# Kernel optimization log

Hardware: AMD Instinct MI355X
Metric: run time of the kernel (lower is better)

Reference implementation:

```python
import jax, jax.numpy as jnp
import numpy as np

EMBED_DIM = 1024
NUM_HEADS = 16
HEAD_DIM = EMBED_DIM // NUM_HEADS
SCALING = HEAD_DIM ** -0.5
TGT_LEN = 2048
BSZ = 2


def setup_inputs() -> dict:
    key = jax.random.key(0)
    ks = jax.random.split(key, 8)
    E = EMBED_DIM
    query = jax.random.normal(ks[0], (TGT_LEN, BSZ, E), dtype=jnp.float32)
    k_in = jax.random.normal(ks[1], (TGT_LEN, BSZ, E), dtype=jnp.float32)
    v_in = jax.random.normal(ks[2], (TGT_LEN, BSZ, E), dtype=jnp.float32)
    attn_mask = jnp.zeros((TGT_LEN, TGT_LEN), dtype=jnp.float32)
    key_padding_mask = jnp.zeros((1, TGT_LEN, TGT_LEN), dtype=jnp.int32)
    # torch.nn.Linear params: y = x @ W.T + b
    lim_qkv = 1.0 / np.sqrt(E)
    W_qkv = jax.random.uniform(ks[3], (3 * E, E), minval=-lim_qkv, maxval=lim_qkv, dtype=jnp.float32)
    b_qkv = jax.random.uniform(ks[4], (3 * E,), minval=-lim_qkv, maxval=lim_qkv, dtype=jnp.float32)
    W_out = jax.random.uniform(ks[5], (E, E), minval=-lim_qkv, maxval=lim_qkv, dtype=jnp.float32)
    b_out = jax.random.uniform(ks[6], (E,), minval=-lim_qkv, maxval=lim_qkv, dtype=jnp.float32)
    return {"query": query, "key": k_in, "value": v_in, "attn_mask": attn_mask,
            "key_padding_mask": key_padding_mask, "W_qkv": W_qkv, "b_qkv": b_qkv,
            "W_out": W_out, "b_out": b_out}


def reference(query, key, value, attn_mask, key_padding_mask, W_qkv, b_qkv, W_out, b_out):
    # NOTE: original module ignores `key`/`value` args (self-attn from query only).
    T, B, E = query.shape
    H, hd = NUM_HEADS, HEAD_DIM
    neg_inf = jnp.float32(-jnp.inf)
    qkv = query @ W_qkv.T + b_qkv                       # [T, B, 3E]
    qkv = jnp.transpose(qkv.reshape(T, B * H, 3 * hd), (1, 0, 2))  # [BH, T, 3hd]
    q, k, v = jnp.split(qkv, 3, axis=-1)                # each [BH, T, hd]
    aw = jnp.einsum('btd,bsd->bts', q, k) * SCALING     # [BH, T, T]
    # quirk of original: exact-zero scores become -inf
    aw = jnp.where(aw == 0, neg_inf, aw)
    am = jnp.where(attn_mask == 0, jnp.float32(0.0), attn_mask * jnp.float32(-10000.0))
    aw = aw + am
    aw = jnp.where(jnp.swapaxes(key_padding_mask, -2, -1) == 0, aw, neg_inf)
    aw = jax.nn.softmax(aw, axis=-1)
    # dropout p=0.0 -> identity
    out = aw @ v                                        # [BH, T, hd]
    # faithful to original: transpose(0,1) then reshape(bsz, tgt_len, E)
    out = jnp.swapaxes(out, 0, 1).reshape(B, T, E)      # [B, T, E]
    return out @ W_out.T + b_out
```

## Files before the change

### kernel.cpp

```cpp
#include <hip/hip_runtime.h>
#include <math.h>

#define TLEN 2048
#define EMB 1024
#define QKVD 3072
#define NROWS 4096
#define LOG2E 1.4426950408889634f

typedef unsigned short u16;
typedef unsigned int u32;
using frag_ab = __attribute__((ext_vector_type(8))) short;
using f32x4   = __attribute__((ext_vector_type(4))) float;

__device__ __forceinline__ u16 f2bf(float x) {
    u32 u = __builtin_bit_cast(u32, x);
    u = (u + 0x7FFFu + ((u >> 16) & 1u)) >> 16;
    return (u16)u;
}

__device__ __forceinline__ u32 cvt_pk_bf16(float lo, float hi) {
    u32 r;
    asm("v_cvt_pk_bf16_f32 %0, %1, %2" : "=v"(r) : "v"(lo), "v"(hi));
    return r;
}

__device__ __forceinline__ float exp2_hw(float x) {
    float r;
    asm("v_exp_f32 %0, %1" : "=v"(r) : "v"(x));
    return r;
}

#define GLL16(g, l) __builtin_amdgcn_global_load_lds(                         \
    (const __attribute__((address_space(1))) void*)(g),                       \
    (__attribute__((address_space(3))) void*)(l), 16, 0, 0)

__global__ __launch_bounds__(256)
void prep(const float* __restrict__ qa, const float* __restrict__ wqkv,
          const float* __restrict__ wout, u16* __restrict__ out,
          const float* __restrict__ am, const int* __restrict__ kpm,
          float* __restrict__ cm, int* __restrict__ flags)
{
    __shared__ int kt[64][65];
    __shared__ int s_any;
    const int tid = threadIdx.x;
    const int bid = blockIdx.x;
    if (bid < 4096) {
        int i = (bid * 256 + tid) * 8;
        const float* src;
        int off;
        if (i < 4194304)      { src = qa;   off = i; }
        else if (i < 7340032) { src = wqkv; off = i - 4194304; }
        else                  { src = wout; off = i - 7340032; }
        float4 x = *reinterpret_cast<const float4*>(src + off);
        float4 y = *reinterpret_cast<const float4*>(src + off + 4);
        union { u16 h[8]; uint4 v; } o;
        o.h[0] = f2bf(x.x); o.h[1] = f2bf(x.y); o.h[2] = f2bf(x.z); o.h[3] = f2bf(x.w);
        o.h[4] = f2bf(y.x); o.h[5] = f2bf(y.y); o.h[6] = f2bf(y.z); o.h[7] = f2bf(y.w);
        *reinterpret_cast<uint4*>(out + i) = o.v;
        return;
    }
    const int id2 = bid - 4096;
    const int s0 = (id2 & 31) * 64, t0 = (id2 >> 5) * 64;
    if (tid == 0) s_any = 0;
    #pragma unroll
    for (int u = 0; u < 4; ++u) {
        int idx = u * 256 + tid;
        int r  = idx >> 4;
        int cq = (idx & 15) * 4;
        int4 v = *reinterpret_cast<const int4*>(&kpm[(size_t)(s0 + r) * TLEN + t0 + cq]);
        kt[r][cq + 0] = v.x; kt[r][cq + 1] = v.y; kt[r][cq + 2] = v.z; kt[r][cq + 3] = v.w;
    }
    __syncthreads();
    float rbuf[4][4];
    int myany = 0;
    #pragma unroll
    for (int u = 0; u < 4; ++u) {
        int idx = u * 256 + tid;
        int r  = idx >> 4;
        int cq = (idx & 15) * 4;
        float4 a = *reinterpret_cast<const float4*>(&am[(size_t)(t0 + r) * TLEN + s0 + cq]);
        const float av[4] = {a.x, a.y, a.z, a.w};
        #pragma unroll
        for (int c = 0; c < 4; ++c) {
            float t = (av[c] == 0.0f) ? 0.0f : av[c] * -10000.0f;
            if (kt[cq + c][r] != 0) t = -INFINITY;
            rbuf[u][c] = t * LOG2E;
            myany |= (rbuf[u][c] != 0.0f);
        }
    }
    if (myany) s_any = 1;
    __syncthreads();
    if (s_any) {
        #pragma unroll
        for (int u = 0; u < 4; ++u) {
            int idx = u * 256 + tid;
            int r  = idx >> 4;
            int cq = (idx & 15) * 4;
            *reinterpret_cast<float4*>(&cm[(size_t)(t0 + r) * TLEN + s0 + cq]) =
                make_float4(rbuf[u][0], rbuf[u][1], rbuf[u][2], rbuf[u][3]);
        }
    }
    if (tid == 0) flags[id2] = s_any;
}

template <int OUT_MODE, int NF>
__global__ __launch_bounds__(256)
void gemm_nt_mfma(const u16* __restrict__ A, const u16* __restrict__ B,
                  const float* __restrict__ bias, void* __restrict__ Cp,
                  u16* __restrict__ Vg, int M, int N, int K)
{
    constexpr int BN = NF * 32;
    __shared__ u16 As[128 * 32];
    __shared__ u16 Bs[BN * 32];
    const int tid  = threadIdx.x;
    const int lane = tid & 63;
    const int w    = tid >> 6;
    const int wr   = w >> 1, wc = w & 1;

    const int nbx = N / BN;
    const int id  = blockIdx.x;
    const int lin = (id & 7) * ((int)gridDim.x >> 3) + (id >> 3);
    const int bm = (lin / nbx) * 128, bn = (lin % nbx) * BN;

    f32x4 acc[4][NF];
    #pragma unroll
    for (int i = 0; i < 4; ++i)
        #pragma unroll
        for (int j = 0; j < NF; ++j)
            acc[i][j] = (f32x4){0.f, 0.f, 0.f, 0.f};

    const int srow = tid >> 2;
    const int skel = (tid & 3) * 8;
    const u16* Ag = A + (size_t)(bm + srow) * K + skel;
    const u16* Bg = B + (size_t)(bn + srow % BN) * K + skel;
    u16* Asl = As + srow * 32 + skel;
    u16* Bsl = Bs + (srow % BN) * 32 + skel;

    const int fr = lane & 15;
    const int fk = (lane >> 4) * 8;

    for (int k0 = 0; k0 < K; k0 += 32) {
        GLL16(Ag + k0, Asl);
        GLL16(Ag + (size_t)64 * K + k0, Asl + 64 * 32);
        GLL16(Bg + k0, Bsl);
        if constexpr (NF == 4) GLL16(Bg + (size_t)64 * K + k0, Bsl + 64 * 32);
        __syncthreads();
        frag_ab af[4], bfr[NF];
        #pragma unroll
        for (int mf = 0; mf < 4; ++mf)
            af[mf] = *reinterpret_cast<const frag_ab*>(&As[(wr * 64 + mf * 16 + fr) * 32 + fk]);
        #pragma unroll
        for (int nf = 0; nf < NF; ++nf)
            bfr[nf] = *reinterpret_cast<const frag_ab*>(
                &Bs[(wc * (NF * 16) + nf * 16 + fr) * 32 + fk]);
        #pragma unroll
        for (int mf = 0; mf < 4; ++mf)
            #pragma unroll
            for (int nf = 0; nf < NF; ++nf)
                acc[mf][nf] = __builtin_amdgcn_mfma_f32_16x16x32_bf16(af[mf], bfr[nf], acc[mf][nf], 0, 0, 0);
        __syncthreads();
    }

    const int col0 = bn + wc * (NF * 16) + fr;
    const int row0 = bm + wr * 64 + (lane >> 4) * 4;
    #pragma unroll
    for (int nf = 0; nf < NF; ++nf) {
        const int col = col0 + nf * 16;
        const float bv = bias[col];
        if constexpr (OUT_MODE == 0) {
            #pragma unroll
            for (int mf = 0; mf < 4; ++mf)
                #pragma unroll
                for (int i = 0; i < 4; ++i)
                    ((float*)Cp)[(size_t)(row0 + mf * 16 + i) * N + col] = acc[mf][nf][i] + bv;
        } else {
            const u32 q6 = (u32)col >> 6;
            const u32 h = (q6 * 0xAAABu) >> 17;
            const int seg = col - (int)h * 192;
            if (seg < 128) {
                #pragma unroll
                for (int mf = 0; mf < 4; ++mf)
                    #pragma unroll
                    for (int i = 0; i < 4; ++i)
                        ((u16*)Cp)[(size_t)(row0 + mf * 16 + i) * N + col] =
                            f2bf(acc[mf][nf][i] + bv);
            } else {
                const int d = seg - 128;
                #pragma unroll
                for (int mf = 0; mf < 4; ++mf)
                    #pragma unroll
                    for (int i = 0; i < 4; ++i) {
                        const int row = row0 + mf * 16 + i;
                        Vg[(size_t)(((row & 1) * 16 + (int)h) * 64 + d) * TLEN + (row >> 1)] =
                            f2bf(acc[mf][nf][i] + bv);
                    }
            }
        }
    }
}

#define SM_KS 8192
#define SM_VT 24576

#define ATTN_STEP(CUR, NXT, IT, ITN)                                          \
  {                                                                           \
    GLL16(kbase + (size_t)(((ITN) * 64 + srow) * 2 + b) * QKVD + gsrc,        \
          smem + SM_KS + (NXT) * 8192 + tid * 16);                            \
    GLL16(kbase + (size_t)(((ITN) * 64 + 32 + srow) * 2 + b) * QKVD + gsrc,   \
          smem + SM_KS + (NXT) * 8192 + 4096 + tid * 16);                     \
    GLL16(vgbase + (size_t)srow * TLEN + (ITN) * 64 + gsrc,                   \
          smem + SM_VT + (NXT) * 8192 + tid * 16);                            \
    GLL16(vgbase + (size_t)(srow + 32) * TLEN + (ITN) * 64 + gsrc,            \
          smem + SM_VT + (NXT) * 8192 + 4096 + tid * 16);                     \
    f32x4 sacc[4];                                                            \
    _Pragma("unroll") for (int nf = 0; nf < 4; ++nf)                          \
      sacc[nf] = (f32x4){0.f, 0.f, 0.f, 0.f};                                 \
    __builtin_amdgcn_s_setprio(1);                                            \
    _Pragma("unroll") for (int nf = 0; nf < 4; ++nf) {                        \
      _Pragma("unroll") for (int ks = 0; ks < 2; ++ks) {                      \
        frag_ab bk = *reinterpret_cast<const frag_ab*>(                       \
            smem + SM_KS + (CUR) * 8192 + nf * 2048 + (ks ? kb1 : kb0));      \
        sacc[nf] = __builtin_amdgcn_mfma_f32_16x16x32_bf16(bk, aq[ks],        \
                                                           sacc[nf], 0, 0, 0); \
      }                                                                       \
    }                                                                         \
    __builtin_amdgcn_s_setprio(0);                                            \
    float vq[4][4];                                                           \
    _Pragma("unroll") for (int nf = 0; nf < 4; ++nf) {                        \
      _Pragma("unroll") for (int i = 0; i < 4; ++i) {                         \
        const float sv = sacc[nf][i];                                         \
        const float v = fmaf(SSCALE, sv, -24.0f);                             \
        vq[nf][i] = (sv == 0.0f) ? -INFINITY : v;                             \
      }                                                                       \
    }                                                                         \
    if (fmask & (1u << (IT))) {                                               \
      _Pragma("unroll") for (int nf = 0; nf < 4; ++nf) {                      \
        const float4 c4 = *reinterpret_cast<const float4*>(                   \
            &cm2[(size_t)rq * TLEN + (IT) * 64 + nf * 16 + 4 * fg]);          \
        vq[nf][0] += c4.x; vq[nf][1] += c4.y;                                 \
        vq[nf][2] += c4.z; vq[nf][3] += c4.w;                                 \
      }                                                                       \
    }                                                                         \
    float pv[4][4];                                                           \
    _Pragma("unroll") for (int nf = 0; nf < 4; ++nf) {                        \
      _Pragma("unroll") for (int i = 0; i < 4; ++i)                           \
        pv[nf][i] = exp2_hw(vq[nf][i]);                                       \
    }                                                                         \
    u32 pkA[4], pkB[4];                                                       \
    _Pragma("unroll") for (int nf = 0; nf < 4; ++nf) {                        \
      pkA[nf] = cvt_pk_bf16(pv[nf][0], pv[nf][1]);                            \
      pkB[nf] = cvt_pk_bf16(pv[nf][2], pv[nf][3]);                            \
    }                                                                         \
    __builtin_amdgcn_s_setprio(1);                                            \
    _Pragma("unroll") for (int ks = 0; ks < 2; ++ks) {                        \
      u32 d0 = pkA[2 * ks], d1 = pkB[2 * ks];                                 \
      u32 s0 = pkA[2 * ks + 1], s1 = pkB[2 * ks + 1];                         \
      asm("v_permlane32_swap_b32 %0, %1" : "+v"(d0), "+v"(s0));               \
      asm("v_permlane32_swap_b32 %0, %1" : "+v"(d1), "+v"(s1));               \
      const u32 sel0 = odd ? d0 : s0;                                         \
      const u32 sel1 = odd ? d1 : s1;                                         \
      const u32 r0_ = __builtin_amdgcn_ds_swizzle(sel0, 0x401F);              \
      const u32 r1_ = __builtin_amdgcn_ds_swizzle(sel1, 0x401F);              \
      union { u32 wq[4]; frag_ab f; } pau;                                    \
      pau.wq[0] = odd ? r0_ : d0;                                             \
      pau.wq[1] = odd ? r1_ : d1;                                             \
      pau.wq[2] = odd ? s0 : r0_;                                             \
      pau.wq[3] = odd ? s1 : r1_;                                             \
      _Pragma("unroll") for (int nf = 0; nf < 4; ++nf) {                      \
        frag_ab bv = *reinterpret_cast<const frag_ab*>(                       \
            smem + SM_VT + (CUR) * 8192 + nf * 2048 + (ks ? kb1 : kb0));      \
        oacc[nf] = __builtin_amdgcn_mfma_f32_16x16x32_bf16(pau.f, bv,         \
                                                           oacc[nf], 0, 0, 0); \
      }                                                                       \
      osum = __builtin_amdgcn_mfma_f32_16x16x32_bf16(pau.f, fones, osum,      \
                                                     0, 0, 0);                \
    }                                                                         \
    __builtin_amdgcn_s_setprio(0);                                            \
    asm volatile("s_waitcnt vmcnt(0)" ::: "memory");                          \
    __builtin_amdgcn_s_barrier();                                             \
  }

__global__ __launch_bounds__(256, 4)
void attn_mfma(const u16* __restrict__ qkv, const float* __restrict__ cm2,
               const int* __restrict__ flags, const u16* __restrict__ Vg,
               u16* __restrict__ X2)
{
    __shared__ __attribute__((aligned(16))) char smem[40960];

    const int tid  = threadIdx.x;
    const int lane = tid & 63;
    const int w    = tid >> 6;

    const int id  = blockIdx.x;
    const int lin = (id & 7) * 128 + (id >> 3);
    const int bh  = lin >> 5;
    const int tt  = lin & 31;
    const int b = bh >> 4, h = bh & 15;
    const int t0 = tt * 64;

    const u16* qbase  = qkv + h * 192;
    const u16* kbase  = qkv + h * 192 + 64;
    const u16* vgbase = Vg + (size_t)bh * 64 * TLEN;

    const int srow = tid >> 3;
    const int sgl  = tid & 7;
    const int gsrc = ((sgl ^ (srow & 7)) & 7) * 8;
    const int fr = lane & 15;
    const int fg = lane >> 4;
    const bool odd = (lane & 16) != 0;
    const int rq = t0 + w * 16 + fr;

    const int kb0 = fr * 128 + (((fg) ^ (fr & 7)) & 7) * 16;
    const int kb1 = fr * 128 + (((4 + fg) ^ (fr & 7)) & 7) * 16;

    frag_ab fones;
    #pragma unroll
    for (int j = 0; j < 8; ++j) fones[j] = (short)0x3F80;

    const int* fl = flags + tt * 32;
    int fv = 0;
    if (lane < 32) fv = fl[lane];
    const u32 fmask = (u32)__ballot(fv != 0);

    GLL16(qbase + (size_t)((t0 + srow) * 2 + b) * QKVD + gsrc, smem + tid * 16);
    GLL16(qbase + (size_t)((t0 + 32 + srow) * 2 + b) * QKVD + gsrc, smem + 4096 + tid * 16);
    GLL16(kbase + (size_t)(srow * 2 + b) * QKVD + gsrc, smem + SM_KS + tid * 16);
    GLL16(kbase + (size_t)((32 + srow) * 2 + b) * QKVD + gsrc, smem + SM_KS + 4096 + tid * 16);
    GLL16(vgbase + (size_t)srow * TLEN + gsrc, smem + SM_VT + tid * 16);
    GLL16(vgbase + (size_t)(srow + 32) * TLEN + gsrc, smem + SM_VT + 4096 + tid * 16);
    __syncthreads();

    frag_ab aq[2];
    aq[0] = *reinterpret_cast<const frag_ab*>(smem + w * 2048 + kb0);
    aq[1] = *reinterpret_cast<const frag_ab*>(smem + w * 2048 + kb1);

    f32x4 oacc[4];
    #pragma unroll
    for (int nf = 0; nf < 4; ++nf) oacc[nf] = (f32x4){0.f, 0.f, 0.f, 0.f};
    f32x4 osum = (f32x4){0.f, 0.f, 0.f, 0.f};

    const float SSCALE = 0.125f * LOG2E;

    for (int it = 0; it < 32; it += 2) {
        const int it1 = it + 1;
        ATTN_STEP(0, 1, it, it1)
        ATTN_STEP(1, 0, it1, (it1 < 31 ? it1 + 1 : 31))
    }

    #pragma unroll
    for (int i = 0; i < 4; ++i) {
        const int t = t0 + w * 16 + fg * 4 + i;
        const int rout = ((t >= 1024) ? 2048 : 0) + 2 * (t & 1023) + b;
        const float inv = 1.f / osum[i];
        #pragma unroll
        for (int nf = 0; nf < 4; ++nf)
            X2[(size_t)rout * EMB + h * 64 + nf * 16 + fr] = f2bf(oacc[nf][i] * inv);
    }
}

extern "C" void kernel_launch(void* const* d_in, const int* in_sizes, int n_in,
                              void* d_out, int out_size, void* d_ws, size_t ws_size,
                              hipStream_t stream)
{
    const float* query = (const float*)d_in[0];
    const float* am    = (const float*)d_in[3];
    const int*   kpm   = (const int*)d_in[4];
    const float* Wqkv  = (const float*)d_in[5];
    const float* bqkv  = (const float*)d_in[6];
    const float* Wout  = (const float*)d_in[7];
    const float* bout  = (const float*)d_in[8];
    float* out = (float*)d_out;

    char* ws = (char*)d_ws;
    u16*   qkv_bf  = (u16*)(ws);
    u16*   x2_bf   = (u16*)(ws + 25165824);
    float* cmask   = (float*)(ws + 33554432);
    u16*   q_bf    = (u16*)(ws + 50331648);
    u16*   wqkv_bf = (u16*)(ws + 58720256);
    u16*   wout_bf = (u16*)(ws + 65011712);
    int*   flags   = (int*)(ws + 67108864);
    u16*   v_tr    = (u16*)(ws + 67112960);

    prep<<<5120, 256, 0, stream>>>(query, Wqkv, Wout, q_bf, am, kpm, cmask, flags);

    gemm_nt_mfma<2, 4><<<768, 256, 0, stream>>>(q_bf, wqkv_bf, bqkv, qkv_bf,
                                                v_tr, NROWS, QKVD, EMB);
    attn_mfma<<<1024, 256, 0, stream>>>(qkv_bf, cmask, flags, v_tr, x2_bf);
    gemm_nt_mfma<0, 2><<<512, 256, 0, stream>>>(x2_bf, wout_bf, bout, out,
                                                nullptr, NROWS, EMB, EMB);
}
```

Baseline: 133.9 us.

## Software-pipeline QK^T scores one tile ahead of softmax and PV

Restructures the attention loop so the QK^T MFMA for the next key tile is issued after the barrier of the current step, while the current step's softmax and PV use scores computed in the previous iteration. Prefetch of the tile two steps ahead is moved after the barrier into the buffer just consumed. The aim is to overlap the exp/convert work with MFMA work and to hide load latency. It costs an extra 16 accumulator registers for the second score set, which may pressure occupancy at 4 blocks per SM.

```diff
diff --git a/kernel.cpp b/kernel.cpp
--- a/kernel.cpp
+++ b/kernel.cpp
@@ -202,33 +202,13 @@
 #define SM_KS 8192
 #define SM_VT 24576
 
-#define ATTN_STEP(CUR, NXT, IT, ITN)                                          \
+#define ATTN_STEP(CUR, NXT, IT, SIN, SOUT)                                    \
   {                                                                           \
-    GLL16(kbase + (size_t)(((ITN) * 64 + srow) * 2 + b) * QKVD + gsrc,        \
-          smem + SM_KS + (NXT) * 8192 + tid * 16);                            \
-    GLL16(kbase + (size_t)(((ITN) * 64 + 32 + srow) * 2 + b) * QKVD + gsrc,   \
-          smem + SM_KS + (NXT) * 8192 + 4096 + tid * 16);                     \
-    GLL16(vgbase + (size_t)srow * TLEN + (ITN) * 64 + gsrc,                   \
-          smem + SM_VT + (NXT) * 8192 + tid * 16);                            \
-    GLL16(vgbase + (size_t)(srow + 32) * TLEN + (ITN) * 64 + gsrc,            \
-          smem + SM_VT + (NXT) * 8192 + 4096 + tid * 16);                     \
-    f32x4 sacc[4];                                                            \
-    _Pragma("unroll") for (int nf = 0; nf < 4; ++nf)                          \
-      sacc[nf] = (f32x4){0.f, 0.f, 0.f, 0.f};                                 \
-    __builtin_amdgcn_s_setprio(1);                                            \
-    _Pragma("unroll") for (int nf = 0; nf < 4; ++nf) {                        \
-      _Pragma("unroll") for (int ks = 0; ks < 2; ++ks) {                      \
-        frag_ab bk = *reinterpret_cast<const frag_ab*>(                       \
-            smem + SM_KS + (CUR) * 8192 + nf * 2048 + (ks ? kb1 : kb0));      \
-        sacc[nf] = __builtin_amdgcn_mfma_f32_16x16x32_bf16(bk, aq[ks],        \
-                                                           sacc[nf], 0, 0, 0); \
-      }                                                                       \
-    }                                                                         \
-    __builtin_amdgcn_s_setprio(0);                                            \
+                    \
     float vq[4][4];                                                           \
     _Pragma("unroll") for (int nf = 0; nf < 4; ++nf) {                        \
       _Pragma("unroll") for (int i = 0; i < 4; ++i) {                         \
-        const float sv = sacc[nf][i];                                         \
+        const float sv = SIN[nf][i];                                          \
         const float v = fmaf(SSCALE, sv, -24.0f);                             \
         vq[nf][i] = (sv == 0.0f) ? -INFINITY : v;                             \
       }                                                                       \
@@ -251,6 +231,7 @@
       pkA[nf] = cvt_pk_bf16(pv[nf][0], pv[nf][1]);                            \
       pkB[nf] = cvt_pk_bf16(pv[nf][2], pv[nf][3]);                            \
     }                                                                         \
+                      \
     __builtin_amdgcn_s_setprio(1);                                            \
     _Pragma("unroll") for (int ks = 0; ks < 2; ++ks) {                        \
       u32 d0 = pkA[2 * ks], d1 = pkB[2 * ks];                                 \
@@ -278,6 +259,31 @@
     __builtin_amdgcn_s_setprio(0);                                            \
     asm volatile("s_waitcnt vmcnt(0)" ::: "memory");                          \
     __builtin_amdgcn_s_barrier();                                             \
+          \
+    {                                                                         \
+      const int itn = ((IT) + 2 < 32) ? (IT) + 2 : 31;                        \
+      GLL16(kbase + (size_t)((itn * 64 + srow) * 2 + b) * QKVD + gsrc,        \
+            smem + SM_KS + (CUR) * 8192 + tid * 16);                          \
+      GLL16(kbase + (size_t)((itn * 64 + 32 + srow) * 2 + b) * QKVD + gsrc,   \
+            smem + SM_KS + (CUR) * 8192 + 4096 + tid * 16);                   \
+      GLL16(vgbase + (size_t)srow * TLEN + itn * 64 + gsrc,                   \
+            smem + SM_VT + (CUR) * 8192 + tid * 16);                          \
+      GLL16(vgbase + (size_t)(srow + 32) * TLEN + itn * 64 + gsrc,            \
+            smem + SM_VT + (CUR) * 8192 + 4096 + tid * 16);                   \
+    }                                                                         \
+     \
+    _Pragma("unroll") for (int nf = 0; nf < 4; ++nf)                          \
+      SOUT[nf] = (f32x4){0.f, 0.f, 0.f, 0.f};                                 \
+    __builtin_amdgcn_s_setprio(1);                                            \
+    _Pragma("unroll") for (int nf = 0; nf < 4; ++nf) {                        \
+      _Pragma("unroll") for (int ks = 0; ks < 2; ++ks) {                      \
+        frag_ab bk = *reinterpret_cast<const frag_ab*>(                       \
+            smem + SM_KS + (NXT) * 8192 + nf * 2048 + (ks ? kb1 : kb0));      \
+        SOUT[nf] = __builtin_amdgcn_mfma_f32_16x16x32_bf16(bk, aq[ks],        \
+                                                           SOUT[nf], 0, 0, 0); \
+      }                                                                       \
+    }                                                                         \
+    __builtin_amdgcn_s_setprio(0);                                            \
   }
 
 __global__ __launch_bounds__(256, 4)
@@ -334,17 +340,37 @@
     aq[0] = *reinterpret_cast<const frag_ab*>(smem + w * 2048 + kb0);
     aq[1] = *reinterpret_cast<const frag_ab*>(smem + w * 2048 + kb1);
 
+    GLL16(kbase + (size_t)((64 + srow) * 2 + b) * QKVD + gsrc, smem + SM_KS + 8192 + tid * 16);
+    GLL16(kbase + (size_t)((96 + srow) * 2 + b) * QKVD + gsrc, smem + SM_KS + 8192 + 4096 + tid * 16);
+    GLL16(vgbase + (size_t)srow * TLEN + 64 + gsrc, smem + SM_VT + 8192 + tid * 16);
+    GLL16(vgbase + (size_t)(srow + 32) * TLEN + 64 + gsrc, smem + SM_VT + 8192 + 4096 + tid * 16);
+
     f32x4 oacc[4];
     #pragma unroll
     for (int nf = 0; nf < 4; ++nf) oacc[nf] = (f32x4){0.f, 0.f, 0.f, 0.f};
     f32x4 osum = (f32x4){0.f, 0.f, 0.f, 0.f};
+    f32x4 saccA[4], saccB[4];
 
     const float SSCALE = 0.125f * LOG2E;
 
+    #pragma unroll
+    for (int nf = 0; nf < 4; ++nf) saccA[nf] = (f32x4){0.f, 0.f, 0.f, 0.f};
+    __builtin_amdgcn_s_setprio(1);
+    #pragma unroll
+    for (int nf = 0; nf < 4; ++nf) {
+        #pragma unroll
+        for (int ks = 0; ks < 2; ++ks) {
+            frag_ab bk = *reinterpret_cast<const frag_ab*>(
+                smem + SM_KS + nf * 2048 + (ks ? kb1 : kb0));
+            saccA[nf] = __builtin_amdgcn_mfma_f32_16x16x32_bf16(bk, aq[ks],
+                                                                saccA[nf], 0, 0, 0);
+        }
+    }
+    __builtin_amdgcn_s_setprio(0);
+
     for (int it = 0; it < 32; it += 2) {
-        const int it1 = it + 1;
-        ATTN_STEP(0, 1, it, it1)
-        ATTN_STEP(1, 0, it1, (it1 < 31 ? it1 + 1 : 31))
+        ATTN_STEP(0, 1, it, saccA, saccB)
+        ATTN_STEP(1, 0, it + 1, saccB, saccA)
     }
 
     #pragma unroll
```

New measurement: 134.2 us. No clear change (+0.3%).
